# Performance work log

Measured on AMD Instinct MI355X. Metric: run time of the kernel, lower is better.

The kernel has to match this reference:

```python
import jax, jax.numpy as jnp
import numpy as np

B, S, HID = 1, 2048, 3072
NH, NKV, HD = 24, 8, 128
SCALING = 128.0 ** -0.5
SOFTCAP = 50.0
EPS = 1e-6
NEG = -1e9


def setup_inputs() -> dict:
    key = jax.random.key(0)
    ks = jax.random.split(key, 8)
    inv_freq = 1.0 / (10000.0 ** (jnp.arange(0, HD, 2, dtype=jnp.float32) / HD))
    pos = jnp.arange(S, dtype=jnp.float32)
    freqs = jnp.outer(pos, inv_freq)                      # [S, HD/2]
    emb = jnp.concatenate([freqs, freqs], axis=-1)        # [S, HD]
    cos = jnp.cos(emb)[None]                              # [B, S, HD]
    sin = jnp.sin(emb)[None]
    causal = jnp.tril(jnp.ones((S, S), dtype=bool))
    attention_mask = jnp.where(causal, 0.0, NEG).astype(jnp.float32)[None, None]  # [1,1,S,S]
    return {
        'hidden_states': jax.random.normal(ks[0], (B, S, HID), jnp.float32),
        'cos': cos,
        'sin': sin,
        'attention_mask': attention_mask,
        'wq': jax.random.normal(ks[1], (NH * HD, HID), jnp.float32) * 0.02,
        'wk': jax.random.normal(ks[2], (NKV * HD, HID), jnp.float32) * 0.02,
        'wv': jax.random.normal(ks[3], (NKV * HD, HID), jnp.float32) * 0.02,
        'wo': jax.random.normal(ks[4], (HID, NH * HD), jnp.float32) * 0.02,
        'q_norm_w': jnp.zeros((HD,), jnp.float32),
        'k_norm_w': jnp.zeros((HD,), jnp.float32),
    }


def _rms_norm(x, w, eps=EPS):
    xf = x.astype(jnp.float32)
    out = xf * jax.lax.rsqrt(jnp.mean(xf * xf, axis=-1, keepdims=True) + eps)
    return (out * (1.0 + w.astype(jnp.float32))).astype(x.dtype)


def _rotate_half(x):
    x1, x2 = jnp.split(x, 2, axis=-1)
    return jnp.concatenate([-x2, x1], axis=-1)


def reference(hidden_states, cos, sin, attention_mask, wq, wk, wv, wo, q_norm_w, k_norm_w):
    b, s, _ = hidden_states.shape
    q = jnp.einsum('bsd,ed->bse', hidden_states, wq).reshape(b, s, NH, HD).transpose(0, 2, 1, 3)
    k = jnp.einsum('bsd,ed->bse', hidden_states, wk).reshape(b, s, NKV, HD).transpose(0, 2, 1, 3)
    v = jnp.einsum('bsd,ed->bse', hidden_states, wv).reshape(b, s, NKV, HD).transpose(0, 2, 1, 3)
    q = _rms_norm(q, q_norm_w)
    k = _rms_norm(k, k_norm_w)
    c = cos[:, None]  # [B,1,S,HD]
    sn = sin[:, None]
    q = q * c + _rotate_half(q) * sn
    k = k * c + _rotate_half(k) * sn
    n_rep = NH // NKV
    k = jnp.repeat(k, n_rep, axis=1)  # [B,NH,S,HD]
    v = jnp.repeat(v, n_rep, axis=1)
    scores = jnp.einsum('bhqd,bhkd->bhqk', q, k) * SCALING
    scores = jnp.tanh(scores / SOFTCAP) * SOFTCAP
    scores = scores + attention_mask
    probs = jax.nn.softmax(scores.astype(jnp.float32), axis=-1).astype(q.dtype)
    out = jnp.einsum('bhqk,bhkd->bhqd', probs, v)
    out = out.transpose(0, 2, 1, 3).reshape(b, s, NH * HD)
    return jnp.einsum('bse,de->bsd', out, wo)
```

## Files before the change

### kernel.cpp

```cpp
#include <hip/hip_runtime.h>
#include <hip/hip_bf16.h>

#define S_LEN 2048
#define HIDV  3072
#define NHQ   24
#define NKVH  8
#define HDIM  128

typedef __bf16 bf16x8 __attribute__((ext_vector_type(8)));
typedef float  f32x4  __attribute__((ext_vector_type(4)));
typedef int    i32x4  __attribute__((ext_vector_type(4)));

__device__ __forceinline__ void gload_lds16(const void* g, void* l) {
    __builtin_amdgcn_global_load_lds((__attribute__((address_space(1))) void*)g,
                                     (__attribute__((address_space(3))) void*)l, 16, 0, 0);
}

__global__ void cast_all(const float* __restrict__ hs, const float* __restrict__ wq,
                         const float* __restrict__ wk, const float* __restrict__ wv,
                         const float* __restrict__ wo,
                         __hip_bfloat16* __restrict__ hsb, __hip_bfloat16* __restrict__ wf,
                         __hip_bfloat16* __restrict__ wob) {
    int c = blockIdx.x * blockDim.x + threadIdx.x;
    const float* src; __hip_bfloat16* dst; int off;
    if (c < 1572864)      { src = hs; dst = hsb;            off = c; }
    else if (c < 3932160) { src = wq; dst = wf;             off = c - 1572864; }
    else if (c < 4718592) { src = wk; dst = wf + 9437184;   off = c - 3932160; }
    else if (c < 5505024) { src = wv; dst = wf + 12582912;  off = c - 4718592; }
    else                  { src = wo; dst = wob;            off = c - 5505024; }
    float4 v = *(const float4*)(src + off * 4);
    union { __hip_bfloat16 h[4]; ushort4 u; } pk;
    pk.h[0] = __float2bfloat16(v.x);
    pk.h[1] = __float2bfloat16(v.y);
    pk.h[2] = __float2bfloat16(v.z);
    pk.h[3] = __float2bfloat16(v.w);
    *(ushort4*)(dst + off * 4) = pk.u;
}

template<int NF, int MODE>
__global__ __launch_bounds__(256) void gemm_tile(const __hip_bfloat16* __restrict__ A,
                                                 const __hip_bfloat16* __restrict__ B,
                                                 void* __restrict__ C0, void* __restrict__ C1,
                                                 void* __restrict__ C2)
{
    __shared__ __hip_bfloat16 As[2][128 * 32];
    __shared__ __hip_bfloat16 Bs[2][NF * 32 * 32];
    const int tid = threadIdx.x;
    const int w    = tid >> 6;
    const int lane = tid & 63;
    const int lr = lane & 15, lg = lane >> 4;
    const int wr = w >> 1, wc = w & 1;

    const int wg = ((int)blockIdx.x & 7) * 64 + ((int)blockIdx.x >> 3);
    const int bn = wg >> 4, bm = wg & 15;

    f32x4 zf = {0.f, 0.f, 0.f, 0.f};
    f32x4 acc[4][NF];
#pragma unroll
    for (int i = 0; i < 4; ++i)
#pragma unroll
        for (int j = 0; j < NF; ++j) acc[i][j] = zf;

    const char* Ab = (const char*)A + (size_t)(bm * 128) * 6144;
    const char* Bb = (const char*)B + (size_t)(bn * NF * 32) * 6144;
    const int NT = 96;

#define GT_STAGE(buf, t) do {                                                       \
        int k0b_ = (t) << 6;                                                        \
        _Pragma("unroll")                                                           \
        for (int u_ = 0; u_ < 2; ++u_) {                                            \
            int u = tid + 256 * u_;                                                 \
            gload_lds16(Ab + (size_t)(u >> 2) * 6144 + k0b_ + (u & 3) * 16,         \
                        (char*)As[buf] + u * 16);                                   \
        }                                                                           \
        _Pragma("unroll")                                                           \
        for (int u_ = 0; u_ < (4 * NF * 32 + 255) / 256; ++u_) {                    \
            int u = tid + 256 * u_;                                                 \
            if ((4 * NF * 32) % 256 == 0 || u < 4 * NF * 32)                        \
                gload_lds16(Bb + (size_t)(u >> 2) * 6144 + k0b_ + (u & 3) * 16,     \
                            (char*)Bs[buf] + u * 16);                               \
        } } while (0)

    GT_STAGE(0, 0);
    __syncthreads();

    for (int t = 0; t < NT; ++t) {
        const int cur = t & 1;
        if (t + 1 < NT) GT_STAGE(cur ^ 1, t + 1);
        bf16x8 af[4], bfr[NF];
#pragma unroll
        for (int i = 0; i < 4; ++i)
            af[i] = *(const bf16x8*)(As[cur] + (wr * 64 + i * 16 + lr) * 32 + lg * 8);
#pragma unroll
        for (int j = 0; j < NF; ++j)
            bfr[j] = *(const bf16x8*)(Bs[cur] + ((wc * NF + j) * 16 + lr) * 32 + lg * 8);
#pragma unroll
        for (int mi = 0; mi < 4; ++mi)
#pragma unroll
            for (int ni = 0; ni < NF; ++ni)
                acc[mi][ni] = __builtin_amdgcn_mfma_f32_16x16x32_bf16(af[mi], bfr[ni], acc[mi][ni], 0, 0, 0);
        __syncthreads();
    }
#undef GT_STAGE

#pragma unroll
    for (int mi = 0; mi < 4; ++mi)
#pragma unroll
        for (int ni = 0; ni < NF; ++ni) {
            int row0 = bm * 128 + wr * 64 + mi * 16 + lg * 4;
            int col  = bn * NF * 32 + wc * NF * 16 + ni * 16 + lr;
            f32x4 v = acc[mi][ni];
            if (MODE == 0) {
#pragma unroll
                for (int j = 0; j < 4; ++j)
                    ((float*)C0)[(size_t)(row0 + j) * 3072 + col] = v[j];
            } else {
                if (col < 3072) {
#pragma unroll
                    for (int j = 0; j < 4; ++j)
                        ((__hip_bfloat16*)C0)[(size_t)(row0 + j) * 3072 + col] = __float2bfloat16(v[j]);
                } else if (col < 4096) {
#pragma unroll
                    for (int j = 0; j < 4; ++j)
                        ((__hip_bfloat16*)C1)[(size_t)(row0 + j) * 1024 + (col - 3072)] = __float2bfloat16(v[j]);
                } else {
                    union { __hip_bfloat16 h[4]; ushort4 u; } pk;
#pragma unroll
                    for (int j = 0; j < 4; ++j) pk.h[j] = __float2bfloat16(v[j]);
                    *(ushort4*)((__hip_bfloat16*)C2 + (size_t)(col - 4096) * 2048 + row0) = pk.u;
                }
            }
        }
}

__global__ void norm_rope_fused(const __hip_bfloat16* __restrict__ qpre,
                                const __hip_bfloat16* __restrict__ kpre,
                                __hip_bfloat16* __restrict__ qb, __hip_bfloat16* __restrict__ kb,
                                const float* __restrict__ qnw, const float* __restrict__ knw,
                                const float* __restrict__ cosp, const float* __restrict__ sinp)
{
    int gw = blockIdx.x * 4 + (threadIdx.x >> 6);
    int lane = threadIdx.x & 63;
    const __hip_bfloat16* row;
    const float* nw;
    __hip_bfloat16* outp;
    int s;
    if (gw < 49152) {
        s = gw / 24; int h = gw - s * 24;
        row  = qpre + (size_t)s * 3072 + h * HDIM;
        outp = qb   + (size_t)s * 3072 + h * HDIM;
        nw = qnw;
    } else {
        int g = gw - 49152;
        s = g >> 3; int h = g & 7;
        row  = kpre + (size_t)s * 1024 + h * HDIM;
        outp = kb + (size_t)h * 262144 + (size_t)s * 128;
        nw = knw;
    }
    float x1 = __bfloat162float(row[lane]), x2 = __bfloat162float(row[lane + 64]);
    float ss = x1 * x1 + x2 * x2;
#pragma unroll
    for (int xm = 1; xm < 64; xm <<= 1) ss += __shfl_xor(ss, xm, 64);
    float rs = rsqrtf(ss * (1.f / 128.f) + 1e-6f);
    float n1 = x1 * rs * (1.f + nw[lane]);
    float n2 = x2 * rs * (1.f + nw[lane + 64]);
    float c1 = cosp[s * HDIM + lane], c2 = cosp[s * HDIM + lane + 64];
    float s1 = sinp[s * HDIM + lane], s2 = sinp[s * HDIM + lane + 64];
    outp[lane]      = __float2bfloat16(n1 * c1 - n2 * s1);
    outp[lane + 64] = __float2bfloat16(n2 * c2 + n1 * s2);
}

__global__ __launch_bounds__(384) void attn_kernel(
    const __hip_bfloat16* __restrict__ Q,
    const __hip_bfloat16* __restrict__ Kc,
    const __hip_bfloat16* __restrict__ Vt,
    __hip_bfloat16* __restrict__ O)
{
    extern __shared__ __align__(16) char smem[];
    const int pb = blockIdx.x;
    const int kh = blockIdx.y;
    const int tid = threadIdx.x;
    const int w = tid >> 6;
    const int lane = tid & 63;
    const int lr = lane & 15, lg = lane >> 4;
    const int h = kh * 3 + (w >> 1);
    const int strip = w & 1;

    const char* kg = (const char*)(Kc + (size_t)kh * S_LEN * HDIM);
    const char* vg = (const char*)(Vt + (size_t)kh * HDIM * S_LEN);
    __hip_bfloat16* pw = (__hip_bfloat16*)(smem + 65536 + w * 2304);

#define ATT_STAGE(b, j0s) do {                                                      \
        if (tid < 256) {                                                            \
            _Pragma("unroll")                                                       \
            for (int i_ = 0; i_ < 4; ++i_) {                                        \
                int base_ = (tid + 256 * i_) * 16;                                  \
                int kr_ = base_ >> 8, kc_ = base_ & 255;                            \
                gload_lds16(kg + (size_t)((j0s) + kr_) * 256 + (kc_ ^ ((kr_ & 7) << 4)), \
                            smem + (b) * 16384 + base_);                            \
                int vr_ = base_ >> 7, vc_ = base_ & 127;                            \
                gload_lds16(vg + (size_t)vr_ * (S_LEN * 2) + (j0s) * 2 + (vc_ ^ ((vr_ & 7) << 4)), \
                            smem + 32768 + (b) * 16384 + base_);                    \
            } } } while (0)

    for (int half = 0; half < 2; ++half) {
        const int hb = half ? (63 - pb) : pb;
        const int q0 = hb * 32;
        const int qrow = q0 + strip * 16;
        const int jtmax = (q0 + 31) >> 6;

        bf16x8 aq[4];
        {
            const __hip_bfloat16* qp = Q + (size_t)(qrow + lr) * HIDV + h * HDIM + lg * 8;
#pragma unroll
            for (int ks = 0; ks < 4; ++ks) aq[ks] = *(const bf16x8*)(qp + ks * 32);
        }

        f32x4 zf = {0.f, 0.f, 0.f, 0.f};
        f32x4 oacc[8];
#pragma unroll
        for (int i = 0; i < 8; ++i) oacc[i] = zf;
        float lacc[4] = {0.f, 0.f, 0.f, 0.f};

        ATT_STAGE(0, 0);
        __syncthreads();

        int buf = 0;
        for (int jt = 0; jt <= jtmax; ++jt) {
            if (jt < jtmax) ATT_STAGE(buf ^ 1, (jt + 1) * 64);

            const int j0 = jt * 64;
            const char* Kb = smem + buf * 16384;
            const char* Vb = smem + 32768 + buf * 16384;

            f32x4 sf[4];
#pragma unroll
            for (int nf = 0; nf < 4; ++nf) {
                sf[nf] = zf;
                int row = nf * 16 + lr;
#pragma unroll
                for (int ks = 0; ks < 4; ++ks) {
                    int boff = (row * 256 + ks * 64 + lg * 16) ^ ((row & 7) << 4);
                    bf16x8 bk = *(const bf16x8*)(Kb + boff);
                    sf[nf] = __builtin_amdgcn_mfma_f32_16x16x32_bf16(aq[ks], bk, sf[nf], 0, 0, 0);
                }
            }

            const bool diag = (jt == jtmax);
#pragma unroll
            for (int nf = 0; nf < 4; ++nf) {
                int jpos = j0 + nf * 16 + lr;
#pragma unroll
                for (int r = 0; r < 4; ++r) {
                    float e2 = __expf(sf[nf][r] * 0.0035355339059327376f);
                    float rr = __builtin_amdgcn_rcpf(e2 + 1.f);
                    float p  = __expf(fmaf(rr, -100.f, 20.f));
                    if (diag && jpos > (qrow + lg * 4 + r)) p = 0.f;
                    lacc[r] += p;
                    pw[(lg * 4 + r) * 72 + nf * 16 + lr] = __float2bfloat16(p);
                }
            }

#pragma unroll
            for (int ks2 = 0; ks2 < 2; ++ks2) {
                bf16x8 ap = *(const bf16x8*)((const char*)pw + lr * 144 + ks2 * 64 + lg * 16);
#pragma unroll
                for (int df = 0; df < 8; ++df) {
                    int row = df * 16 + lr;
                    int boff = (row * 128 + ks2 * 64 + lg * 16) ^ ((row & 7) << 4);
                    bf16x8 bv = *(const bf16x8*)(Vb + boff);
                    oacc[df] = __builtin_amdgcn_mfma_f32_16x16x32_bf16(ap, bv, oacc[df], 0, 0, 0);
                }
            }
            __syncthreads();
            buf ^= 1;
        }

#pragma unroll
        for (int r = 0; r < 4; ++r) {
            float t = lacc[r];
#pragma unroll
            for (int xm = 1; xm < 16; xm <<= 1) t += __shfl_xor(t, xm, 64);
            float inv = __builtin_amdgcn_rcpf(t);
            size_t rowoff = (size_t)(qrow + lg * 4 + r) * HIDV + h * HDIM;
#pragma unroll
            for (int df = 0; df < 8; ++df)
                O[rowoff + df * 16 + lr] = __float2bfloat16(oacc[df][r] * inv);
        }
    }
#undef ATT_STAGE
}

extern "C" void kernel_launch(void* const* d_in, const int* in_sizes, int n_in,
                              void* d_out, int out_size, void* d_ws, size_t ws_size,
                              hipStream_t stream) {
    const float* hs   = (const float*)d_in[0];
    const float* cosp = (const float*)d_in[1];
    const float* sinp = (const float*)d_in[2];
    const float* wq  = (const float*)d_in[4];
    const float* wk  = (const float*)d_in[5];
    const float* wv  = (const float*)d_in[6];
    const float* wo  = (const float*)d_in[7];
    const float* qnw = (const float*)d_in[8];
    const float* knw = (const float*)d_in[9];
    float* out = (float*)d_out;

    char* ws = (char*)d_ws;
    __hip_bfloat16* hsb  = (__hip_bfloat16*)(ws + 0);
    __hip_bfloat16* wf   = (__hip_bfloat16*)(ws + 12582912);
    __hip_bfloat16* wob  = (__hip_bfloat16*)(ws + 44040192);
    __hip_bfloat16* qpre = (__hip_bfloat16*)(ws + 62914560);
    __hip_bfloat16* kpre = (__hip_bfloat16*)(ws + 75497472);
    __hip_bfloat16* qb   = (__hip_bfloat16*)(ws + 79691776);
    __hip_bfloat16* kb   = (__hip_bfloat16*)(ws + 92274688);
    __hip_bfloat16* vbt  = (__hip_bfloat16*)(ws + 96468992);
    __hip_bfloat16* ob   = (__hip_bfloat16*)(ws + 100663296);

    cast_all<<<30720, 256, 0, stream>>>(hs, wq, wk, wv, wo, hsb, wf, wob);

    gemm_tile<5, 1><<<512, 256, 0, stream>>>(hsb, wf, qpre, kpre, vbt);

    norm_rope_fused<<<16384, 256, 0, stream>>>(qpre, kpre, qb, kb, qnw, knw, cosp, sinp);

    attn_kernel<<<dim3(32, 8), 384, 79360, stream>>>(qb, kb, vbt, ob);

    gemm_tile<3, 0><<<512, 256, 0, stream>>>(ob, wob, out, (void*)0, (void*)0);
}
```

Before: 246.7 us.

## Double GEMM K-tile to 64 and XOR-swizzle LDS layout

The two projection GEMMs now load a K-slice of 64 bf16 per stage instead of 32, which halves the number of main-loop iterations and barriers. Shared memory moves to a dynamic buffer with an XOR swizzle of 16-byte chunks keyed on row, aimed at avoiding LDS bank conflicts on the fragment reads. The larger dynamic LDS footprint (72KB and 56KB) may cut occupancy.

```diff
diff --git a/kernel.cpp b/kernel.cpp
--- a/kernel.cpp
+++ b/kernel.cpp
@@ -43,8 +43,7 @@
                                                  void* __restrict__ C0, void* __restrict__ C1,
                                                  void* __restrict__ C2)
 {
-    __shared__ __hip_bfloat16 As[2][128 * 32];
-    __shared__ __hip_bfloat16 Bs[2][NF * 32 * 32];
+    extern __shared__ __align__(16) char smem[];
     const int tid = threadIdx.x;
     const int w    = tid >> 6;
     const int lane = tid & 63;
@@ -63,22 +62,23 @@
 
     const char* Ab = (const char*)A + (size_t)(bm * 128) * 6144;
     const char* Bb = (const char*)B + (size_t)(bn * NF * 32) * 6144;
-    const int NT = 96;
+    const int NT = 48;
 
 #define GT_STAGE(buf, t) do {                                                       \
-        int k0b_ = (t) << 6;                                                        \
+        int k0b_ = (t) << 7;                                                        \
         _Pragma("unroll")                                                           \
-        for (int u_ = 0; u_ < 2; ++u_) {                                            \
+        for (int u_ = 0; u_ < 4; ++u_) {                                            \
             int u = tid + 256 * u_;                                                 \
-            gload_lds16(Ab + (size_t)(u >> 2) * 6144 + k0b_ + (u & 3) * 16,         \
-                        (char*)As[buf] + u * 16);                                   \
+            int r_ = u >> 3, o_ = (u & 7) * 16;                                     \
+            gload_lds16(Ab + (size_t)r_ * 6144 + k0b_ + (o_ ^ ((r_ & 7) << 4)),     \
+                        smem + (buf) * 16384 + u * 16);                             \
         }                                                                           \
         _Pragma("unroll")                                                           \
-        for (int u_ = 0; u_ < (4 * NF * 32 + 255) / 256; ++u_) {                    \
+        for (int u_ = 0; u_ < NF; ++u_) {                                           \
             int u = tid + 256 * u_;                                                 \
-            if ((4 * NF * 32) % 256 == 0 || u < 4 * NF * 32)                        \
-                gload_lds16(Bb + (size_t)(u >> 2) * 6144 + k0b_ + (u & 3) * 16,     \
-                            (char*)Bs[buf] + u * 16);                               \
+            int r_ = u >> 3, o_ = (u & 7) * 16;                                     \
+            gload_lds16(Bb + (size_t)r_ * 6144 + k0b_ + (o_ ^ ((r_ & 7) << 4)),     \
+                        smem + 32768 + (buf) * (NF * 4096) + u * 16);               \
         } } while (0)
 
     GT_STAGE(0, 0);
@@ -87,18 +87,32 @@
     for (int t = 0; t < NT; ++t) {
         const int cur = t & 1;
         if (t + 1 < NT) GT_STAGE(cur ^ 1, t + 1);
-        bf16x8 af[4], bfr[NF];
-#pragma unroll
-        for (int i = 0; i < 4; ++i)
-            af[i] = *(const bf16x8*)(As[cur] + (wr * 64 + i * 16 + lr) * 32 + lg * 8);
-#pragma unroll
-        for (int j = 0; j < NF; ++j)
-            bfr[j] = *(const bf16x8*)(Bs[cur] + ((wc * NF + j) * 16 + lr) * 32 + lg * 8);
+        bf16x8 af[4][2], bfr[NF][2];
+#pragma unroll
+        for (int i = 0; i < 4; ++i) {
+            int row = wr * 64 + i * 16 + lr;
+#pragma unroll
+            for (int kk = 0; kk < 2; ++kk) {
+                int cb = (kk * 64 + lg * 16) ^ ((row & 7) << 4);
+                af[i][kk] = *(const bf16x8*)(smem + cur * 16384 + row * 128 + cb);
+            }
+        }
+#pragma unroll
+        for (int j = 0; j < NF; ++j) {
+            int row = (wc * NF + j) * 16 + lr;
+#pragma unroll
+            for (int kk = 0; kk < 2; ++kk) {
+                int cb = (kk * 64 + lg * 16) ^ ((row & 7) << 4);
+                bfr[j][kk] = *(const bf16x8*)(smem + 32768 + cur * (NF * 4096) + row * 128 + cb);
+            }
+        }
 #pragma unroll
         for (int mi = 0; mi < 4; ++mi)
 #pragma unroll
             for (int ni = 0; ni < NF; ++ni)
-                acc[mi][ni] = __builtin_amdgcn_mfma_f32_16x16x32_bf16(af[mi], bfr[ni], acc[mi][ni], 0, 0, 0);
+#pragma unroll
+                for (int kk = 0; kk < 2; ++kk)
+                    acc[mi][ni] = __builtin_amdgcn_mfma_f32_16x16x32_bf16(af[mi][kk], bfr[ni][kk], acc[mi][ni], 0, 0, 0);
         __syncthreads();
     }
 #undef GT_STAGE
@@ -318,11 +332,11 @@
 
     cast_all<<<30720, 256, 0, stream>>>(hs, wq, wk, wv, wo, hsb, wf, wob);
 
-    gemm_tile<5, 1><<<512, 256, 0, stream>>>(hsb, wf, qpre, kpre, vbt);
+    gemm_tile<5, 1><<<512, 256, 73728, stream>>>(hsb, wf, qpre, kpre, vbt);
 
     norm_rope_fused<<<16384, 256, 0, stream>>>(qpre, kpre, qb, kb, qnw, knw, cosp, sinp);
 
     attn_kernel<<<dim3(32, 8), 384, 79360, stream>>>(qb, kb, vbt, ob);
 
-    gemm_tile<3, 0><<<512, 256, 0, stream>>>(ob, wob, out, (void*)0, (void*)0);
-}
+    gemm_tile<3, 0><<<512, 256, 57344, stream>>>(ob, wob, out, (void*)0, (void*)0);
+}
```

Result: faster. 219.2 us (-11.1%).
